# Performance work log

Measured on AMD Instinct MI355X. Metric: run time of the kernel, lower is better.

Reference implementation:

```python
import jax, jax.numpy as jnp
import numpy as np

NUM_EXPERTS = 8
D_MODEL = 768
D_FF = 4 * D_MODEL


def setup_inputs() -> dict:
    key = jax.random.key(0)
    ks = jax.random.split(key, 7)
    s = 0.02
    x = jax.random.normal(ks[0], (2, 1024, D_MODEL), dtype=jnp.float32)
    router_w = jax.random.normal(ks[1], (D_MODEL, NUM_EXPERTS), dtype=jnp.float32) * s
    router_b = jnp.zeros((NUM_EXPERTS,), dtype=jnp.float32)
    w1 = jax.random.normal(ks[2], (NUM_EXPERTS, D_MODEL, D_FF), dtype=jnp.float32) * s
    b1 = jnp.zeros((NUM_EXPERTS, D_FF), dtype=jnp.float32)
    w2 = jax.random.normal(ks[3], (NUM_EXPERTS, D_FF, D_MODEL), dtype=jnp.float32) * s
    b2 = jnp.zeros((NUM_EXPERTS, D_MODEL), dtype=jnp.float32)
    return {"x": x, "router_w": router_w, "router_b": router_b,
            "w1": w1, "b1": b1, "w2": w2, "b2": b2}


def reference(x, router_w, router_b, w1, b1, w2, b2):
    B, S, D = x.shape
    x_flat = x.reshape(-1, D)                      # [T, D]
    logits = x_flat @ router_w + router_b          # [T, E]
    probs = jax.nn.softmax(logits, axis=-1)
    expert_idx = jnp.argmax(probs, axis=-1)        # [T] int, top-1 routing
    onehot = jax.nn.one_hot(expert_idx, NUM_EXPERTS, dtype=x.dtype)  # [T, E]

    # Per-expert FFN; combine via top-1 one-hot (output is NOT scaled by prob,
    # matching the original). Dropout is eval-mode identity.
    out = jnp.zeros_like(x_flat)
    for e in range(NUM_EXPERTS):
        h = jax.nn.relu(x_flat @ w1[e] + b1[e])    # [T, D_FF]
        y = h @ w2[e] + b2[e]                      # [T, D]
        out = out + onehot[:, e:e + 1] * y
    outputs = out.reshape(B, S, D)

    # Load-balance loss: MSE between empirical expert usage and uniform.
    usage = jnp.bincount(expert_idx, length=NUM_EXPERTS).astype(jnp.float32)
    usage = usage / usage.sum()
    uniform = jnp.full((NUM_EXPERTS,), 1.0 / NUM_EXPERTS, dtype=jnp.float32)
    load_balance_loss = jnp.mean((usage - uniform) ** 2)
    return outputs, load_balance_loss
```

## Files before the change

kernel.cpp:

```cpp
#include <hip/hip_runtime.h>
#include <hip/hip_bf16.h>

#define NTOK 2048
#define DMODEL 768
#define DFF 3072
#define NEXP 8
#define MAXT 40

typedef short bf16x8 __attribute__((ext_vector_type(8)));
typedef float f32x4 __attribute__((ext_vector_type(4)));

typedef __attribute__((address_space(1))) const char GCHAR;
typedef __attribute__((address_space(3))) char LCHAR;
#define GL16(g, l) __builtin_amdgcn_global_load_lds((GCHAR*)(g), (LCHAR*)(l), 16, 0, 0)

template <int K, int N>
__device__ void transpose_tile(const float* __restrict__ W, __hip_bfloat16* __restrict__ WT,
                               int e, int k0, int n0, float* T) {
  const int t = threadIdx.x;
  {
    const int kr = t >> 4;
    const int nc = (t & 15) * 4;
    const float* src = W + ((size_t)e * K + k0) * N + n0;
#pragma unroll
    for (int i = 0; i < 4; i++) {
      float4 v = *(const float4*)(src + (size_t)(kr + i * 16) * N + nc);
      T[(kr + i * 16) * 65 + nc + 0] = v.x;
      T[(kr + i * 16) * 65 + nc + 1] = v.y;
      T[(kr + i * 16) * 65 + nc + 2] = v.z;
      T[(kr + i * 16) * 65 + nc + 3] = v.w;
    }
  }
  __syncthreads();
  {
    const int n = t >> 2;
    const int kq = (t & 3) * 16;
    __align__(16) __hip_bfloat16 u[16];
#pragma unroll
    for (int j = 0; j < 16; j++) u[j] = __float2bfloat16(T[(kq + j) * 65 + n]);
    __hip_bfloat16* dst = WT + ((size_t)e * N + n0 + n) * K + k0 + kq;
    *(int4*)dst = *(const int4*)&u[0];
    *(int4*)(dst + 8) = *(const int4*)&u[8];
  }
}

__global__ __launch_bounds__(256) void k_router_t1(
    const float* __restrict__ x, const float* __restrict__ rw,
    const float* __restrict__ rb, __hip_bfloat16* __restrict__ xbf,
    int* __restrict__ eidx, int* __restrict__ cnt,
    const float* __restrict__ w1, __hip_bfloat16* __restrict__ wT1) {
  __shared__ float T[64 * 65];
  if (blockIdx.x >= 512) {
    int tb = blockIdx.x - 512;
    int n_i = tb % (DFF / 64);
    int k_i = (tb / (DFF / 64)) % (DMODEL / 64);
    int e = tb / ((DFF / 64) * (DMODEL / 64));
    transpose_tile<DMODEL, DFF>(w1, wT1, e, k_i * 64, n_i * 64, T);
    return;
  }
  int tok = (blockIdx.x * blockDim.x + threadIdx.x) >> 6;
  int lane = threadIdx.x & 63;
  if (tok >= NTOK) return;
  const float* xr = x + (size_t)tok * DMODEL;
  double acc[NEXP];
#pragma unroll
  for (int e = 0; e < NEXP; e++) acc[e] = 0.0;
  for (int d0 = 0; d0 < DMODEL; d0 += 64) {
    float v = xr[d0 + lane];
    xbf[(size_t)tok * DMODEL + d0 + lane] = __float2bfloat16(v);
    const float* wrow = rw + (size_t)(d0 + lane) * NEXP;
#pragma unroll
    for (int e = 0; e < NEXP; e++) acc[e] += (double)v * (double)wrow[e];
  }
#pragma unroll
  for (int e = 0; e < NEXP; e++) {
    double a = acc[e];
#pragma unroll
    for (int s = 32; s > 0; s >>= 1) a += __shfl_xor(a, s);
    acc[e] = a;
  }
  if (lane == 0) {
    int best = 0;
    double bv = acc[0] + (double)rb[0];
#pragma unroll
    for (int e = 1; e < NEXP; e++) {
      double v = acc[e] + (double)rb[e];
      if (v > bv) { bv = v; best = e; }
    }
    eidx[tok] = best;
    atomicAdd(&cnt[best], 1);
  }
}

__global__ void k_scan(const int* __restrict__ cnt, int* __restrict__ off,
                       int* __restrict__ cur, float* __restrict__ loss,
                       int* __restrict__ tiles, int* __restrict__ ntile) {
  if (threadIdx.x == 0) {
    int s = 0;
    float l = 0.f;
    int nt = 0;
    for (int e = 0; e < NEXP; e++) {
      off[e] = s;
      cur[e] = s;
      for (int m = 0; m < cnt[e]; m += 64) tiles[nt++] = (e << 20) | m;
      s += cnt[e];
      float u = (float)cnt[e] / (float)NTOK - 1.0f / (float)NEXP;
      l += u * u;
    }
    *ntile = nt;
    *loss = l / (float)NEXP;
  }
}

__global__ __launch_bounds__(256) void k_build(const int* __restrict__ eidx,
                                               int* __restrict__ cur,
                                               int* __restrict__ list) {
  int t = blockIdx.x * blockDim.x + threadIdx.x;
  if (t < NTOK) {
    int e = eidx[t];
    int p = atomicAdd(&cur[e], 1);
    list[p] = t;
  }
}

template <int K_TOT, int KCHUNK, int N, int NSPLIT, bool RELU_BF16, bool GATHER_A,
          bool ATOMIC_C, int TK, int TN>
__global__ __launch_bounds__(256, 6) void k_gemm10(
    const __hip_bfloat16* __restrict__ A, const __hip_bfloat16* __restrict__ BT,
    const float* __restrict__ bias, void* __restrict__ Cout,
    const int* __restrict__ cnt, const int* __restrict__ off,
    const int* __restrict__ list, const int* __restrict__ tiles,
    const int* __restrict__ ntile, const float* __restrict__ Tsrc,
    __hip_bfloat16* __restrict__ Tdst) {
  constexpr int NX = N / 128;
  constexpr int W = NX * MAXT * NSPLIT;
  constexpr int NT = KCHUNK / 32;
  __shared__ __align__(16) char smem[24576];

  if constexpr (TK > 0) {
    if (blockIdx.x >= W) {
      int tb = blockIdx.x - W;
      int n_i = tb % (TN / 64);
      int k_i = (tb / (TN / 64)) % (TK / 64);
      int e = tb / ((TN / 64) * (TK / 64));
      transpose_tile<TK, TN>(Tsrc, Tdst, e, k_i * 64, n_i * 64, (float*)smem);
      return;
    }
  }

  int b = blockIdx.x;
  constexpr int q = W / 8, r = W % 8;
  const int xcd = b & 7, ii = b >> 3;
  const int widx = (xcd < r ? xcd * (q + 1) : r * (q + 1) + (xcd - r) * q) + ii;
  const int split = widx % NSPLIT;
  const int rest = widx / NSPLIT;
  const int ti = rest % MAXT;
  const int nx = rest / MAXT;
  if (ti >= *ntile) return;
  const int tv = tiles[ti];
  const int e = tv >> 20;
  const int m0 = tv & 0xFFFFF;
  const int ce = cnt[e];
  const int oe = off[e];
  const int n0 = nx * 128;
  const int kbase = split * KCHUNK;

  const int tid = threadIdx.x;
  const int lane = tid & 63;
  const int w = tid >> 6;
  const int wr = (w >> 1) * 32;
  const int wc = (w & 1) * 64;
  const int fr = lane & 15;
  const int hi = lane >> 4;
  const int xr = (fr >> 1) & 3;

  const int srow = tid >> 2;
  const int cch = (tid & 3) ^ ((tid >> 3) & 3);

  const __hip_bfloat16* ga;
  {
    int mr = m0 + srow;
    int src;
    if (GATHER_A) {
      src = list[oe + (mr < ce ? mr : 0)];
    } else {
      int p2 = oe + mr;
      src = p2 < NTOK ? p2 : NTOK - 1;
    }
    ga = A + (size_t)src * K_TOT + kbase + cch * 8;
  }
  const __hip_bfloat16* gb[2];
#pragma unroll
  for (int j = 0; j < 2; j++) {
    int nr = n0 + j * 64 + srow;
    gb[j] = BT + ((size_t)e * N + nr) * K_TOT + kbase + cch * 8;
  }

  f32x4 acc[2][4] = {};

#define STAGE(buf, kc)                                              \
  do {                                                              \
    GL16(ga + (kc), smem + (buf)*4096 + tid * 16);                  \
    GL16(gb[0] + (kc), smem + 8192 + (buf)*8192 + tid * 16);        \
    GL16(gb[1] + (kc), smem + 8192 + (buf)*8192 + 4096 + tid * 16); \
  } while (0)

  STAGE(0, 0);
#pragma unroll 1
  for (int t = 0; t < NT; ++t) {
    if (t + 1 < NT) {
      STAGE((t + 1) & 1, (t + 1) * 32);
      asm volatile("s_waitcnt vmcnt(3)" ::: "memory");
    } else {
      asm volatile("s_waitcnt vmcnt(0)" ::: "memory");
    }
    __builtin_amdgcn_s_barrier();
    {
      const char* bA = smem + (t & 1) * 4096;
      const char* bB = smem + 8192 + (t & 1) * 8192;
      bf16x8 fa[2], fb[4];
#pragma unroll
      for (int mf = 0; mf < 2; mf++) {
        const int row = wr + mf * 16 + fr;
        fa[mf] = *(const bf16x8*)(bA + row * 64 + ((hi ^ xr) * 16));
      }
#pragma unroll
      for (int nf = 0; nf < 4; nf++) {
        const int row = wc + nf * 16 + fr;
        fb[nf] = *(const bf16x8*)(bB + row * 64 + ((hi ^ xr) * 16));
      }
#pragma unroll
      for (int mf = 0; mf < 2; mf++)
#pragma unroll
        for (int nf = 0; nf < 4; nf++)
          acc[mf][nf] = __builtin_amdgcn_mfma_f32_16x16x32_bf16(fa[mf], fb[nf],
                                                                acc[mf][nf], 0, 0, 0);
    }
    __builtin_amdgcn_s_barrier();
  }
#undef STAGE

#pragma unroll
  for (int mf = 0; mf < 2; mf++) {
#pragma unroll
    for (int jj = 0; jj < 4; jj++) {
      const int mloc = m0 + wr + mf * 16 + hi * 4 + jj;
      if (mloc >= ce) continue;
      if (RELU_BF16) {
        __hip_bfloat16* C = (__hip_bfloat16*)Cout;
        size_t row = (size_t)(oe + mloc) * N;
        const float* bi = bias + (size_t)e * N;
#pragma unroll
        for (int nf = 0; nf < 4; nf++) {
          int nn = n0 + wc + nf * 16 + fr;
          float v = acc[mf][nf][jj] + bi[nn];
          C[row + nn] = __float2bfloat16(v > 0.f ? v : 0.f);
        }
      } else {
        float* C = (float*)Cout;
        int tok = list[oe + mloc];
        size_t row = (size_t)tok * N;
        const float* bi = bias + (size_t)e * N;
#pragma unroll
        for (int nf = 0; nf < 4; nf++) {
          int nn = n0 + wc + nf * 16 + fr;
          float v = acc[mf][nf][jj] + (split == 0 ? bi[nn] : 0.f);
          if (ATOMIC_C)
            atomicAdd(&C[row + nn], v);
          else
            C[row + nn] = v;
        }
      }
    }
  }
}

template <int K, int N, bool RELU_BF16, bool GATHER_A, bool SCATTER_C>
__global__ __launch_bounds__(256) void k_gemm(
    const __hip_bfloat16* __restrict__ A, const float* __restrict__ Bw,
    const float* __restrict__ bias, void* __restrict__ Cout,
    const int* __restrict__ cnt, const int* __restrict__ off,
    const int* __restrict__ list) {
  const int e = blockIdx.z;
  const int ce = cnt[e];
  const int m0 = blockIdx.y * 128;
  if (m0 >= ce) return;
  const int oe = off[e];
  const int n0 = blockIdx.x * 128;

  __shared__ __hip_bfloat16 Asm[128][32];
  __shared__ __hip_bfloat16 Bsm[128][32];

  const int tid = threadIdx.x;
  const int ra = tid >> 1;
  const int ha = (tid & 1) * 16;
  size_t arow;
  {
    int mr = m0 + ra;
    int src;
    if (GATHER_A) {
      src = (mr < ce) ? list[oe + mr] : list[oe];
    } else {
      int p = oe + mr;
      src = (p < NTOK) ? p : (NTOK - 1);
    }
    arow = (size_t)src * K;
  }
  const int rbk = tid >> 3;
  const int nb = (tid & 7) * 16;
  const float* bsrc0 = Bw + ((size_t)e * K + rbk) * N + n0 + nb;

  const int w = tid >> 6;
  const int lane = tid & 63;
  const int wr = (w >> 1) * 64;
  const int wc = (w & 1) * 64;
  const int fr = lane & 15;
  const int fk = (lane >> 4) * 8;

  f32x4 acc[4][4] = {};

  for (int k0 = 0; k0 < K; k0 += 32) {
    __syncthreads();
    {
      const __hip_bfloat16* s = A + arow + k0 + ha;
      int4 v0 = *(const int4*)(s);
      int4 v1 = *(const int4*)(s + 8);
      *(int4*)(&Asm[ra][ha]) = v0;
      *(int4*)(&Asm[ra][ha + 8]) = v1;
    }
    {
      const float* s = bsrc0 + (size_t)k0 * N;
      float4 q0 = *(const float4*)(s);
      float4 q1 = *(const float4*)(s + 4);
      float4 q2 = *(const float4*)(s + 8);
      float4 q3 = *(const float4*)(s + 12);
      __hip_bfloat16* dst = &Bsm[nb][0] + rbk;
      dst[0 * 32] = __float2bfloat16(q0.x);
      dst[1 * 32] = __float2bfloat16(q0.y);
      dst[2 * 32] = __float2bfloat16(q0.z);
      dst[3 * 32] = __float2bfloat16(q0.w);
      dst[4 * 32] = __float2bfloat16(q1.x);
      dst[5 * 32] = __float2bfloat16(q1.y);
      dst[6 * 32] = __float2bfloat16(q1.z);
      dst[7 * 32] = __float2bfloat16(q1.w);
      dst[8 * 32] = __float2bfloat16(q2.x);
      dst[9 * 32] = __float2bfloat16(q2.y);
      dst[10 * 32] = __float2bfloat16(q2.z);
      dst[11 * 32] = __float2bfloat16(q2.w);
      dst[12 * 32] = __float2bfloat16(q3.x);
      dst[13 * 32] = __float2bfloat16(q3.y);
      dst[14 * 32] = __float2bfloat16(q3.z);
      dst[15 * 32] = __float2bfloat16(q3.w);
    }
    __syncthreads();

    bf16x8 fa[4], fb[4];
#pragma unroll
    for (int mf = 0; mf < 4; mf++) fa[mf] = *(const bf16x8*)(&Asm[wr + mf * 16 + fr][fk]);
#pragma unroll
    for (int nf = 0; nf < 4; nf++) fb[nf] = *(const bf16x8*)(&Bsm[wc + nf * 16 + fr][fk]);
#pragma unroll
    for (int mf = 0; mf < 4; mf++)
#pragma unroll
      for (int nf = 0; nf < 4; nf++)
        acc[mf][nf] = __builtin_amdgcn_mfma_f32_16x16x32_bf16(fa[mf], fb[nf], acc[mf][nf], 0, 0, 0);
  }

#pragma unroll
  for (int mf = 0; mf < 4; mf++) {
#pragma unroll
    for (int j = 0; j < 4; j++) {
      const int mloc = m0 + wr + mf * 16 + (lane >> 4) * 4 + j;
      if (mloc >= ce) continue;
      if (RELU_BF16) {
        __hip_bfloat16* C = (__hip_bfloat16*)Cout;
        size_t row = (size_t)(oe + mloc) * N;
        const float* bi = bias + (size_t)e * N;
#pragma unroll
        for (int nf = 0; nf < 4; nf++) {
          int nn = n0 + wc + nf * 16 + fr;
          float v = acc[mf][nf][j] + bi[nn];
          C[row + nn] = __float2bfloat16(v > 0.f ? v : 0.f);
        }
      } else {
        float* C = (float*)Cout;
        int tok = SCATTER_C ? list[oe + mloc] : (oe + mloc);
        size_t row = (size_t)tok * N;
        const float* bi = bias + (size_t)e * N;
#pragma unroll
        for (int nf = 0; nf < 4; nf++) {
          int nn = n0 + wc + nf * 16 + fr;
          C[row + nn] = acc[mf][nf][j] + bi[nn];
        }
      }
    }
  }
}

extern "C" void kernel_launch(void* const* d_in, const int* in_sizes, int n_in,
                              void* d_out, int out_size, void* d_ws, size_t ws_size,
                              hipStream_t stream) {
  const float* x = (const float*)d_in[0];
  const float* rw = (const float*)d_in[1];
  const float* rb = (const float*)d_in[2];
  const float* w1 = (const float*)d_in[3];
  const float* b1 = (const float*)d_in[4];
  const float* w2 = (const float*)d_in[5];
  const float* b2 = (const float*)d_in[6];
  float* out = (float*)d_out;

  char* ws = (char*)d_ws;
  int* cnt = (int*)(ws + 0);
  int* off = (int*)(ws + 32);
  int* cur = (int*)(ws + 64);
  int* ntile = (int*)(ws + 96);
  int* tiles = (int*)(ws + 128);
  int* eidx = (int*)(ws + 512);
  int* list = (int*)(ws + 8704);
  __hip_bfloat16* xbf = (__hip_bfloat16*)(ws + 65536);
  __hip_bfloat16* h = (__hip_bfloat16*)(ws + 4194304);
  __hip_bfloat16* wT1 = (__hip_bfloat16*)(ws + 20971520);
  __hip_bfloat16* wT2 = (__hip_bfloat16*)(ws + 58720256);

  float* loss = out + (size_t)2 * 1024 * 768;
  const size_t REQ = 58720256ull + 37748736ull;

  (void)hipMemsetAsync(cnt, 0, 96, stream);
  (void)hipMemsetAsync(d_out, 0, (size_t)out_size * sizeof(float), stream);

  if (ws_size >= REQ) {
    const int TBLK = (DMODEL / 64) * (DFF / 64) * NEXP;
    k_router_t1<<<512 + TBLK, 256, 0, stream>>>(x, rw, rb, xbf, eidx, cnt, w1, wT1);
    k_scan<<<1, 64, 0, stream>>>(cnt, off, cur, loss, tiles, ntile);
    k_build<<<8, 256, 0, stream>>>(eidx, cur, list);
    k_gemm10<DMODEL, DMODEL, DFF, 1, true, true, false, DFF, DMODEL>
        <<<(DFF / 128) * MAXT + TBLK, 256, 0, stream>>>(
            xbf, wT1, b1, h, cnt, off, list, tiles, ntile, w2, wT2);
    k_gemm10<DFF, DFF / 4, DMODEL, 4, false, false, true, 0, 64>
        <<<(DMODEL / 128) * MAXT * 4, 256, 0, stream>>>(
            h, wT2, b2, out, cnt, off, list, tiles, ntile, nullptr, nullptr);
  } else {
    k_router_t1<<<512, 256, 0, stream>>>(x, rw, rb, xbf, eidx, cnt, w1, nullptr);
    k_scan<<<1, 64, 0, stream>>>(cnt, off, cur, loss, tiles, ntile);
    k_build<<<8, 256, 0, stream>>>(eidx, cur, list);
    k_gemm<DMODEL, DFF, true, true, false>
        <<<dim3(DFF / 128, 16, NEXP), 256, 0, stream>>>(xbf, w1, b1, h, cnt, off, list);
    k_gemm<DFF, DMODEL, false, false, true>
        <<<dim3(DMODEL / 128, 16, NEXP), 256, 0, stream>>>(h, w2, b2, out, cnt, off, list);
  }
}
```

Before: 148.8 us.

## Merge scan/build kernels and replace split-K atomics with partial buffers plus reduce

Fuses the scan and list-build kernels into a single one-block kernel that uses a shared-memory cursor, removing one launch. The second GEMM now writes split-K partial sums into separate workspace slices, which reuse the wT1 region since it is dead by then, instead of doing float atomicAdd into the output. A new reduce kernel sums the four partials and adds the expert bias, so the output memset is no longer needed. The trade is an extra kernel launch and extra partial-buffer traffic in place of atomic contention, and the result becomes deterministic.

```diff
diff --git a/kernel.cpp b/kernel.cpp
--- a/kernel.cpp
+++ b/kernel.cpp
@@ -92,16 +92,18 @@
   }
 }
 
-__global__ void k_scan(const int* __restrict__ cnt, int* __restrict__ off,
-                       int* __restrict__ cur, float* __restrict__ loss,
-                       int* __restrict__ tiles, int* __restrict__ ntile) {
+__global__ __launch_bounds__(256) void k_scanbuild(
+    const int* __restrict__ cnt, int* __restrict__ off, float* __restrict__ loss,
+    int* __restrict__ tiles, int* __restrict__ ntile,
+    const int* __restrict__ eidx, int* __restrict__ list) {
+  __shared__ int s_cur[NEXP];
   if (threadIdx.x == 0) {
     int s = 0;
     float l = 0.f;
     int nt = 0;
     for (int e = 0; e < NEXP; e++) {
       off[e] = s;
-      cur[e] = s;
+      s_cur[e] = s;
       for (int m = 0; m < cnt[e]; m += 64) tiles[nt++] = (e << 20) | m;
       s += cnt[e];
       float u = (float)cnt[e] / (float)NTOK - 1.0f / (float)NEXP;
@@ -110,22 +112,17 @@
     *ntile = nt;
     *loss = l / (float)NEXP;
   }
-}
-
-__global__ __launch_bounds__(256) void k_build(const int* __restrict__ eidx,
-                                               int* __restrict__ cur,
-                                               int* __restrict__ list) {
-  int t = blockIdx.x * blockDim.x + threadIdx.x;
-  if (t < NTOK) {
+  __syncthreads();
+  for (int t = threadIdx.x; t < NTOK; t += 256) {
     int e = eidx[t];
-    int p = atomicAdd(&cur[e], 1);
+    int p = atomicAdd(&s_cur[e], 1);
     list[p] = t;
   }
 }
 
 template <int K_TOT, int KCHUNK, int N, int NSPLIT, bool RELU_BF16, bool GATHER_A,
-          bool ATOMIC_C, int TK, int TN>
-__global__ __launch_bounds__(256, 6) void k_gemm10(
+          int TK, int TN>
+__global__ __launch_bounds__(256, 6) void k_gemm9(
     const __hip_bfloat16* __restrict__ A, const __hip_bfloat16* __restrict__ BT,
     const float* __restrict__ bias, void* __restrict__ Cout,
     const int* __restrict__ cnt, const int* __restrict__ off,
@@ -259,20 +256,37 @@
       } else {
         float* C = (float*)Cout;
         int tok = list[oe + mloc];
-        size_t row = (size_t)tok * N;
-        const float* bi = bias + (size_t)e * N;
+        size_t row = ((size_t)split * NTOK + tok) * N;
 #pragma unroll
         for (int nf = 0; nf < 4; nf++) {
           int nn = n0 + wc + nf * 16 + fr;
-          float v = acc[mf][nf][jj] + (split == 0 ? bi[nn] : 0.f);
-          if (ATOMIC_C)
-            atomicAdd(&C[row + nn], v);
-          else
-            C[row + nn] = v;
+          C[row + nn] = acc[mf][nf][jj];
         }
       }
     }
   }
+}
+
+__global__ __launch_bounds__(256) void k_reduce(const float* __restrict__ p,
+                                                const float* __restrict__ b2,
+                                                const int* __restrict__ eidx,
+                                                float* __restrict__ out) {
+  const int idx = blockIdx.x * 256 + threadIdx.x;
+  const int base = idx * 4;
+  const int tok = base / DMODEL;
+  const int n = base - tok * DMODEL;
+  const int e = eidx[tok];
+  float4 a = *(const float4*)(p + (size_t)0 * NTOK * DMODEL + base);
+  float4 c = *(const float4*)(p + (size_t)1 * NTOK * DMODEL + base);
+  float4 d = *(const float4*)(p + (size_t)2 * NTOK * DMODEL + base);
+  float4 g = *(const float4*)(p + (size_t)3 * NTOK * DMODEL + base);
+  float4 bb = *(const float4*)(b2 + (size_t)e * DMODEL + n);
+  float4 o;
+  o.x = a.x + c.x + d.x + g.x + bb.x;
+  o.y = a.y + c.y + d.y + g.y + bb.y;
+  o.z = a.z + c.z + d.z + g.z + bb.z;
+  o.w = a.w + c.w + d.w + g.w + bb.w;
+  *(float4*)(out + base) = o;
 }
 
 template <int K, int N, bool RELU_BF16, bool GATHER_A, bool SCATTER_C>
@@ -412,7 +426,6 @@
   char* ws = (char*)d_ws;
   int* cnt = (int*)(ws + 0);
   int* off = (int*)(ws + 32);
-  int* cur = (int*)(ws + 64);
   int* ntile = (int*)(ws + 96);
   int* tiles = (int*)(ws + 128);
   int* eidx = (int*)(ws + 512);
@@ -420,29 +433,30 @@
   __hip_bfloat16* xbf = (__hip_bfloat16*)(ws + 65536);
   __hip_bfloat16* h = (__hip_bfloat16*)(ws + 4194304);
   __hip_bfloat16* wT1 = (__hip_bfloat16*)(ws + 20971520);
+  float* part = (float*)(ws + 20971520);
   __hip_bfloat16* wT2 = (__hip_bfloat16*)(ws + 58720256);
 
   float* loss = out + (size_t)2 * 1024 * 768;
   const size_t REQ = 58720256ull + 37748736ull;
 
   (void)hipMemsetAsync(cnt, 0, 96, stream);
-  (void)hipMemsetAsync(d_out, 0, (size_t)out_size * sizeof(float), stream);
+  if (ws_size < REQ)
+    (void)hipMemsetAsync(d_out, 0, (size_t)out_size * sizeof(float), stream);
 
   if (ws_size >= REQ) {
     const int TBLK = (DMODEL / 64) * (DFF / 64) * NEXP;
     k_router_t1<<<512 + TBLK, 256, 0, stream>>>(x, rw, rb, xbf, eidx, cnt, w1, wT1);
-    k_scan<<<1, 64, 0, stream>>>(cnt, off, cur, loss, tiles, ntile);
-    k_build<<<8, 256, 0, stream>>>(eidx, cur, list);
-    k_gemm10<DMODEL, DMODEL, DFF, 1, true, true, false, DFF, DMODEL>
+    k_scanbuild<<<1, 256, 0, stream>>>(cnt, off, loss, tiles, ntile, eidx, list);
+    k_gemm9<DMODEL, DMODEL, DFF, 1, true, true, DFF, DMODEL>
         <<<(DFF / 128) * MAXT + TBLK, 256, 0, stream>>>(
             xbf, wT1, b1, h, cnt, off, list, tiles, ntile, w2, wT2);
-    k_gemm10<DFF, DFF / 4, DMODEL, 4, false, false, true, 0, 64>
+    k_gemm9<DFF, DFF / 4, DMODEL, 4, false, false, 0, 64>
         <<<(DMODEL / 128) * MAXT * 4, 256, 0, stream>>>(
-            h, wT2, b2, out, cnt, off, list, tiles, ntile, nullptr, nullptr);
+            h, wT2, nullptr, part, cnt, off, list, tiles, ntile, nullptr, nullptr);
+    k_reduce<<<(NTOK * DMODEL) / 1024, 256, 0, stream>>>(part, b2, eidx, out);
   } else {
     k_router_t1<<<512, 256, 0, stream>>>(x, rw, rb, xbf, eidx, cnt, w1, nullptr);
-    k_scan<<<1, 64, 0, stream>>>(cnt, off, cur, loss, tiles, ntile);
-    k_build<<<8, 256, 0, stream>>>(eidx, cur, list);
+    k_scanbuild<<<1, 256, 0, stream>>>(cnt, off, loss, tiles, ntile, eidx, list);
     k_gemm<DMODEL, DFF, true, true, false>
         <<<dim3(DFF / 128, 16, NEXP), 256, 0, stream>>>(xbf, w1, b1, h, cnt, off, list);
     k_gemm<DFF, DMODEL, false, false, true>
```

New measurement: 126.5 us, median of 2. 15.0% less time.
